# Kernel optimization log

Measured on AMD Instinct MI355X. Metric: run time of the kernel, lower is better.

The kernel has to match this reference:

```python
import jax, jax.numpy as jnp
import numpy as np

B = 8192      # batch (nodes)
HOPS = 15
SEQ = HOPS + 1
IN = 512      # input_dim
H = 256       # hidden_dim
DS = 64       # d_state
L = 6         # n_layers
NC = 40       # n_class
EPS = 1e-5


def _ln(x, g, b):
    m = x.mean(-1, keepdims=True)
    v = x.var(-1, keepdims=True)  # population var, matches torch LayerNorm
    return (x - m) / jnp.sqrt(v + EPS) * g + b


def setup_inputs() -> dict:
    key = jax.random.key(0)
    ks = jax.random.split(key, 16)
    n = lambda k, shp: jax.random.normal(k, shp, dtype=jnp.float32) * 0.02
    inp = {}
    inp["batched_data"] = jax.random.normal(ks[0], (B, SEQ, IN), dtype=jnp.float32)
    inp["in_w"] = n(ks[1], (H, IN)); inp["in_b"] = jnp.zeros((H,), jnp.float32)
    # per-layer stacked params (leading dim L); note: each MambaBlock shares ONE
    # LayerNorm instance for both pre-ssm and pre-ffn norm.
    inp["norm_g"] = jnp.ones((L, H), jnp.float32); inp["norm_b"] = jnp.zeros((L, H), jnp.float32)
    inp["A_w"] = n(ks[2], (L, DS, H))
    inp["B_w"] = n(ks[3], (L, DS, H))
    inp["C_w"] = n(ks[4], (L, H, DS))
    inp["D_w"] = n(ks[5], (L, H, H)); inp["D_b"] = jnp.zeros((L, H), jnp.float32)
    inp["gate_w"] = n(ks[6], (L, H, H)); inp["gate_b"] = jnp.zeros((L, H), jnp.float32)
    inp["ffn_w1"] = n(ks[7], (L, 2 * H, H)); inp["ffn_b1"] = jnp.zeros((L, 2 * H), jnp.float32)
    inp["ffn_w2"] = n(ks[8], (L, H, 2 * H)); inp["ffn_b2"] = jnp.zeros((L, H), jnp.float32)
    inp["fln_g"] = jnp.ones((H,), jnp.float32); inp["fln_b"] = jnp.zeros((H,), jnp.float32)
    inp["out_w"] = n(ks[9], (H // 2, H)); inp["out_b"] = jnp.zeros((H // 2,), jnp.float32)
    inp["cls_w"] = n(ks[10], (NC, H // 2)); inp["cls_b"] = jnp.zeros((NC,), jnp.float32)
    inp["attn_w"] = n(ks[11], (1, 2 * H)); inp["attn_b"] = jnp.zeros((1,), jnp.float32)
    return inp


def reference(batched_data, in_w, in_b, norm_g, norm_b, A_w, B_w, C_w, D_w, D_b,
              gate_w, gate_b, ffn_w1, ffn_b1, ffn_w2, ffn_b2, fln_g, fln_b,
              out_w, out_b, cls_w, cls_b, attn_w, attn_b):
    x = batched_data @ in_w.T + in_b  # [B,S,H]

    def layer(x, p):
        ng, nb, Aw, Bw, Cw, Dw, Db, gw, gb, w1, b1, w2, b2 = p
        y = _ln(x, ng, nb)
        # precompute all per-step projections in batched GEMMs
        a = jnp.tanh(jnp.einsum('bsh,dh->bsd', y, Aw))   # [B,S,DS]
        bt = jnp.einsum('bsh,dh->bsd', y, Bw)            # [B,S,DS]
        g = jax.nn.sigmoid(y @ gw.T + gb)                # [B,S,H]
        dt = y @ Dw.T + Db                               # [B,S,H]

        def step(h, ab):
            at, bbt = ab
            h = at * h + bbt
            return h, h

        h0 = jnp.zeros((x.shape[0], Aw.shape[0]), x.dtype)
        _, hs = jax.lax.scan(step, h0, (a.transpose(1, 0, 2), bt.transpose(1, 0, 2)))  # [S,B,DS]
        ys = jnp.einsum('sbd,hd->bsh', hs, Cw)           # [B,S,H]
        x = x + ys * g + dt * (1.0 - g)
        y = _ln(x, ng, nb)  # same norm params (shared LayerNorm in block)
        y = jax.nn.gelu(y @ w1.T + b1, approximate=False) @ w2.T + b2
        return x + y, None

    x, _ = jax.lax.scan(layer, x, (norm_g, norm_b, A_w, B_w, C_w, D_w, D_b,
                                   gate_w, gate_b, ffn_w1, ffn_b1, ffn_w2, ffn_b2))
    x = _ln(x, fln_g, fln_b)
    node = x[:, :1, :]           # [B,1,H]
    nbr = x[:, 1:, :]            # [B,S-1,H]
    ai = jnp.concatenate([jnp.broadcast_to(node, nbr.shape), nbr], axis=2)  # [B,S-1,2H]
    aw = jax.nn.softmax(ai @ attn_w.T + attn_b, axis=1)  # [B,S-1,1]
    agg = jnp.sum(nbr * aw, axis=1, keepdims=True)
    out = (node + agg)[:, 0, :]
    out = jax.nn.relu(out @ out_w.T + out_b) @ cls_w.T + cls_b
    return jax.nn.log_softmax(out, axis=1)
```

## Files before the change

### kernel.cpp

```cpp
#include <hip/hip_runtime.h>

typedef __attribute__((ext_vector_type(8))) short bf16x8_t;
typedef __attribute__((ext_vector_type(4))) float f32x4_t;

__device__ __forceinline__ ushort f2bf(float x) {
  union { float f; unsigned u; } a; a.f = x;
  unsigned r = a.u + 0x7fffu + ((a.u >> 16) & 1u);
  return (ushort)(r >> 16);
}
__device__ __forceinline__ float bf2f(ushort s) {
  union { unsigned u; float f; } a; a.u = ((unsigned)s) << 16;
  return a.f;
}
__device__ __forceinline__ void gload_lds16(const void* g, void* l) {
  __builtin_amdgcn_global_load_lds(
      (const __attribute__((address_space(1))) unsigned int*)g,
      (__attribute__((address_space(3))) unsigned int*)l, 16, 0, 0);
}
__device__ __forceinline__ int swzkey(int r) { return ((r >> 2) ^ r) & 3; }

__global__ void cvt_kernel(const float* __restrict__ s, ushort* __restrict__ d, int n) {
  int i = blockIdx.x * 256 + threadIdx.x;
  if (i < n) d[i] = f2bf(s[i]);
}

__global__ void build_wcat(const float* __restrict__ Aw, const float* __restrict__ Bw,
                           const float* __restrict__ gw, const float* __restrict__ Dw,
                           ushort* __restrict__ out) {
  int i = blockIdx.x * 256 + threadIdx.x;
  if (i >= 6 * 640 * 256) return;
  int l = i / (640 * 256), r = (i / 256) % 640, c = i % 256;
  float v;
  if (r < 64)        v = Aw[((l * 64 + r) * 256) + c];
  else if (r < 128)  v = Bw[((l * 64 + (r - 64)) * 256) + c];
  else if (r < 384)  v = gw[((l * 256 + (r - 128)) * 256) + c];
  else               v = Dw[((l * 256 + (r - 384)) * 256) + c];
  out[i] = f2bf(v);
}

__global__ void repack_gen(const ushort* __restrict__ src, ushort* __restrict__ dst,
                           int K, int perMat, int dstPerMat, int dstOff, long total) {
  const long i = (long)blockIdx.x * 256 + threadIdx.x;
  if (i >= total) return;
  const int m = (int)(i / perMat);
  const int idx = (int)(i % perMat);
  const int slice = idx >> 12;
  const int ksn = K >> 5;
  const int p = slice / ksn, ks = slice - p * ksn;
  const int r = (idx >> 5) & 127;
  const int s = (idx >> 3) & 3;
  const int e = idx & 7;
  const int k = ks * 32 + ((s ^ ((r >> 1) & 3)) << 3) + e;
  dst[(long)m * dstPerMat + dstOff + idx] = src[(long)m * perMat + (p * 128 + r) * K + k];
}

__global__ __launch_bounds__(256, 3)
void mamba_fused(ushort* __restrict__ y, ushort* __restrict__ xP,
                 const ushort* __restrict__ Wk,
                 const float* __restrict__ gb, const float* __restrict__ db,
                 const float* __restrict__ lng, const float* __restrict__ lnb) {
  __shared__ __align__(16) char WsB[2 * 16384];
  __shared__ __align__(16) ushort ab[32 * 136];
  __shared__ __align__(16) char HsB[4096];
  __shared__ float lsum[32][2], lsq[32][2];

  const int t = threadIdx.x, lane = t & 63, wid = t >> 6;
  const long m0 = (long)blockIdx.x * 32;
  const int wr = (wid >> 1) * 16, wc = (wid & 1) * 64;
  const int co4 = wid * 4;
  const char* Wb = (const char*)Wk;

  const int krow = lane & 15, kslot = lane >> 4;
  const int ar = wr + krow;

  bf16x8_t afr[8];
  {
    const char* yrow = (const char*)y + (m0 + ar) * 512 + kslot * 16;
#pragma unroll
    for (int ks = 0; ks < 8; ++ks) afr[ks] = *(const bf16x8_t*)(yrow + ks * 64);
  }
#pragma unroll
  for (int c = 0; c < 4; ++c)
    gload_lds16(Wb + (co4 + c) * 1024 + lane * 16, WsB + (co4 + c) * 1024);

  int boff[4];
#pragma unroll
  for (int i = 0; i < 4; ++i) {
    const int br = wc + i * 16 + krow;
    boff[i] = br * 64 + ((kslot ^ ((br >> 1) & 3)) << 4);
  }
  const int rbase = (lane >> 4) * 4, cbase = lane & 15;

  const f32x4_t zero = {0.f, 0.f, 0.f, 0.f};
  f32x4_t acc[4];
#pragma unroll
  for (int i = 0; i < 4; ++i) acc[i] = zero;

  int pair = 0;
  auto kstep2 = [&](bf16x8_t afa, bf16x8_t afb) {
    __syncthreads();
    if (pair + 1 < 22) {
      const char* src = Wb + (long)(pair + 1) * 16384;
      char* dst = WsB + ((pair + 1) & 1) * 16384;
#pragma unroll
      for (int c = 0; c < 4; ++c)
        gload_lds16(src + (co4 + c) * 1024 + lane * 16, dst + (co4 + c) * 1024);
    }
    const char* Wc = WsB + (pair & 1) * 16384;
    bf16x8_t bva[4], bvb[4];
#pragma unroll
    for (int i = 0; i < 4; ++i) bva[i] = *(const bf16x8_t*)(Wc + boff[i]);
#pragma unroll
    for (int i = 0; i < 4; ++i) bvb[i] = *(const bf16x8_t*)(Wc + 8192 + boff[i]);
    __builtin_amdgcn_s_setprio(1);
#pragma unroll
    for (int ni = 0; ni < 4; ++ni)
      acc[ni] = __builtin_amdgcn_mfma_f32_16x16x32_bf16(afa, bva[ni], acc[ni], 0, 0, 0);
#pragma unroll
    for (int ni = 0; ni < 4; ++ni)
      acc[ni] = __builtin_amdgcn_mfma_f32_16x16x32_bf16(afb, bvb[ni], acc[ni], 0, 0, 0);
    __builtin_amdgcn_s_setprio(0);
    ++pair;
  };

#pragma unroll
  for (int p = 0; p < 4; ++p) kstep2(afr[2 * p], afr[2 * p + 1]);
#pragma unroll
  for (int ni = 0; ni < 4; ++ni) {
    const int col = wc + ni * 16 + cbase;
#pragma unroll
    for (int j = 0; j < 4; ++j) {
      const int row = wr + rbase + j;
      const float v = acc[ni][j];
      ab[row * 136 + col] = f2bf(col < 64 ? tanhf(v) : v);
    }
    acc[ni] = zero;
  }
  __syncthreads();
  if (t < 128) {
    const int b = t >> 6, d = t & 63;
    float av[16], btv[16];
#pragma unroll
    for (int s = 0; s < 16; ++s) {
      const int row = b * 16 + s;
      av[s]  = bf2f(ab[row * 136 + d]);
      btv[s] = bf2f(ab[row * 136 + 64 + d]);
    }
    float h = 0.f;
#pragma unroll
    for (int s = 0; s < 16; ++s) {
      h = fmaf(av[s], h, btv[s]);
      const int row = b * 16 + s;
      *(ushort*)(HsB + row * 128 + (((d >> 3) ^ (row & 7)) << 4) + (d & 7) * 2) = f2bf(h);
    }
  }

  f32x4_t gsv[2][4], dsv[2][4], xnv[2][4];
#pragma unroll
  for (int pp = 0; pp < 2; ++pp) {
#pragma unroll
    for (int p = 0; p < 4; ++p) kstep2(afr[2 * p], afr[2 * p + 1]);
#pragma unroll
    for (int ni = 0; ni < 4; ++ni) {
      const int col = pp * 128 + wc + ni * 16 + cbase;
#pragma unroll
      for (int j = 0; j < 4; ++j) {
        const float s = acc[ni][j] + gb[col];
        gsv[pp][ni][j] = 1.f / (1.f + expf(-s));
      }
      acc[ni] = zero;
    }
  }
#pragma unroll
  for (int pp = 0; pp < 2; ++pp) {
#pragma unroll
    for (int p = 0; p < 4; ++p) kstep2(afr[2 * p], afr[2 * p + 1]);
#pragma unroll
    for (int ni = 0; ni < 4; ++ni) {
      const int col = pp * 128 + wc + ni * 16 + cbase;
#pragma unroll
      for (int j = 0; j < 4; ++j) dsv[pp][ni][j] = acc[ni][j] + db[col];
      acc[ni] = zero;
    }
  }
  const long rq16 = (m0 >> 4) + (wr >> 4);
#pragma unroll
  for (int pp = 0; pp < 2; ++pp) {
    const bf16x8_t afh0 = *(const bf16x8_t*)(
        HsB + (ar << 7) + ((kslot ^ (ar & 7)) << 4));
    const bf16x8_t afh1 = *(const bf16x8_t*)(
        HsB + (ar << 7) + (((4 | kslot) ^ (ar & 7)) << 4));
    kstep2(afh0, afh1);
#pragma unroll
    for (int ni = 0; ni < 4; ++ni) {
      const int colq = pp * 8 + (wid & 1) * 4 + ni;
      const ushort4 x4 = *(const ushort4*)(xP + (rq16 * 16 + colq) * 256 + lane * 4);
#pragma unroll
      for (int j = 0; j < 4; ++j) {
        const float g = gsv[pp][ni][j], dv = dsv[pp][ni][j];
        const float xo = bf2f(j == 0 ? x4.x : (j == 1 ? x4.y : (j == 2 ? x4.z : x4.w)));
        xnv[pp][ni][j] = xo + acc[ni][j] * g + dv * (1.f - g);
      }
      acc[ni] = zero;
    }
  }
#pragma unroll
  for (int j = 0; j < 4; ++j) {
    float ps = 0.f, pq = 0.f;
#pragma unroll
    for (int pp = 0; pp < 2; ++pp)
#pragma unroll
      for (int ni = 0; ni < 4; ++ni) { const float v = xnv[pp][ni][j]; ps += v; pq += v * v; }
#pragma unroll
    for (int off = 1; off < 16; off <<= 1) {
      ps += __shfl_xor(ps, off, 64);
      pq += __shfl_xor(pq, off, 64);
    }
    if ((lane & 15) == 0) {
      const int row = wr + rbase + j;
      lsum[row][wid & 1] = ps;
      lsq[row][wid & 1] = pq;
    }
  }
  __syncthreads();
#pragma unroll
  for (int pp = 0; pp < 2; ++pp) {
#pragma unroll
    for (int ni = 0; ni < 4; ++ni) {
      const int colq = pp * 8 + (wid & 1) * 4 + ni;
      ushort4 o4;
      o4.x = f2bf(xnv[pp][ni][0]);
      o4.y = f2bf(xnv[pp][ni][1]);
      o4.z = f2bf(xnv[pp][ni][2]);
      o4.w = f2bf(xnv[pp][ni][3]);
      *(ushort4*)(xP + (rq16 * 16 + colq) * 256 + lane * 4) = o4;
    }
  }
#pragma unroll
  for (int j = 0; j < 4; ++j) {
    const int row = wr + rbase + j;
    const float sm = lsum[row][0] + lsum[row][1];
    const float q = lsq[row][0] + lsq[row][1];
    const float mean = sm * (1.f / 256.f);
    const float rstd = rsqrtf(q * (1.f / 256.f) - mean * mean + 1e-5f);
#pragma unroll
    for (int pp = 0; pp < 2; ++pp)
#pragma unroll
      for (int ni = 0; ni < 4; ++ni) {
        const int col = pp * 128 + wc + ni * 16 + cbase;
        *(ushort*)(WsB + row * 512 + col * 2) =
            f2bf((xnv[pp][ni][j] - mean) * rstd * lng[col] + lnb[col]);
      }
  }
  __syncthreads();
#pragma unroll
  for (int rr = 0; rr < 4; ++rr) {
    const int byte = rr * 4096 + t * 16;
    const int row = byte >> 9, off = byte & 511;
    const bf16x8_t v = *(const bf16x8_t*)(WsB + byte);
    *(bf16x8_t*)((char*)y + (m0 + row) * 512 + off) = v;
  }
}

template <int NP, int MODE>
__global__ __launch_bounds__(256)
void gemm_ws(const ushort* __restrict__ A, const ushort* __restrict__ Wks,
             const float* __restrict__ b1, ushort* __restrict__ outp) {
  constexpr int KS = 8;
  constexpr int N = NP * 128;
  constexpr int T = NP * KS;
  __shared__ __align__(16) char AsB[128 * 512];

  const int t = threadIdx.x, lane = t & 63, wid = t >> 6;
  const long m0 = (long)blockIdx.x * 128;
  const int wr = (wid >> 1) * 64, wc = (wid & 1) * 64;
  const char* Ab = (const char*)A;
  const char* Wb = (const char*)Wks;

  {
    const int arow = lane >> 5;
    const int aps  = lane & 31;
#pragma unroll
    for (int j = 0; j < 16; ++j) {
      const int r = j * 8 + wid * 2 + arow;
      gload_lds16(Ab + (m0 + r) * 512 + (long)((aps ^ (r & 7)) << 4),
                  AsB + (j * 8 + wid * 2) * 512);
    }
  }

  const int krow = lane & 15, kslot = lane >> 4;
  int abase[4], akey[4], boff[4];
#pragma unroll
  for (int i = 0; i < 4; ++i) {
    const int ar = wr + i * 16 + krow;
    abase[i] = ar * 512;
    akey[i] = ar & 7;
    const int br = wc + i * 16 + krow;
    boff[i] = br * 64 + ((kslot ^ ((br >> 1) & 3)) << 4);
  }

  const f32x4_t zero = {0.f, 0.f, 0.f, 0.f};
  f32x4_t acc[4][4];
#pragma unroll
  for (int i = 0; i < 4; ++i)
#pragma unroll
    for (int j = 0; j < 4; ++j) acc[i][j] = zero;

  const int rbase = (lane >> 4) * 4, cbase = lane & 15;

  __syncthreads();

  bf16x8_t bv[4];
#pragma unroll
  for (int i = 0; i < 4; ++i) bv[i] = *(const bf16x8_t*)(Wb + boff[i]);

  for (int tau = 0; tau < T; ++tau) {
    bf16x8_t bw[4];
    if (tau + 1 < T) {
      const char* src = Wb + (long)(tau + 1) * 8192;
#pragma unroll
      for (int i = 0; i < 4; ++i) bw[i] = *(const bf16x8_t*)(src + boff[i]);
    } else {
#pragma unroll
      for (int i = 0; i < 4; ++i) bw[i] = bv[i];
    }
    const int ks = tau & 7;
    bf16x8_t af[4];
#pragma unroll
    for (int i = 0; i < 4; ++i)
      af[i] = *(const bf16x8_t*)(AsB + abase[i] + ((((ks << 2) | kslot) ^ akey[i]) << 4));
    __builtin_amdgcn_s_setprio(1);
#pragma unroll
    for (int mi = 0; mi < 4; ++mi)
#pragma unroll
      for (int ni = 0; ni < 4; ++ni)
        acc[mi][ni] = __builtin_amdgcn_mfma_f32_16x16x32_bf16(af[mi], bv[ni], acc[mi][ni], 0, 0, 0);
    __builtin_amdgcn_s_setprio(0);
#pragma unroll
    for (int i = 0; i < 4; ++i) bv[i] = bw[i];

    if (ks == KS - 1) {
      const int np = tau >> 3;
#pragma unroll
      for (int mi = 0; mi < 4; ++mi) {
#pragma unroll
        for (int ni = 0; ni < 4; ++ni) {
          const int col = np * 128 + wc + ni * 16 + cbase;
#pragma unroll
          for (int j = 0; j < 4; ++j) {
            const long row = m0 + wr + mi * 16 + rbase + j;
            float s = acc[mi][ni][j] + b1[col];
            float o;
            if constexpr (MODE == 2) o = 0.5f * s * (1.f + erff(s * 0.70710678118654752f));
            else                     o = fmaxf(s, 0.f);
            outp[row * N + col] = f2bf(o);
          }
          acc[mi][ni] = zero;
        }
      }
    }
  }
}

template <int K, int MODE, bool AFP32>
__global__ __launch_bounds__(512)
void gemm_ln(const void* __restrict__ Ap, const ushort* __restrict__ W,
             const float* __restrict__ b1, ushort* __restrict__ xP,
             const float* __restrict__ lng, const float* __restrict__ lnb,
             ushort* __restrict__ y, int writex) {
  constexpr int KS = K / 32;
  __shared__ __align__(16) char WsB[2 * 16384];
  __shared__ __align__(16) char AsB[2 * 8192];
  __shared__ float lsum4[128][4], lsq4[128][4];

  const int t = threadIdx.x, lane = t & 63, wid = t >> 6;
  const int wr = (wid >> 2) * 64, wc = (wid & 3) * 64;
  const int lr = lane >> 2, lc = lane & 3;
  const int ra = wid * 16 + lr;
  const int slog = lc ^ swzkey(ra);
  const int saA = slog << 4;
  const int rw0 = wid * 32 + lr, rw1 = rw0 + 16;
  const int sw0 = (lc ^ swzkey(rw0)) << 4;
  const int sw1 = (lc ^ swzkey(rw1)) << 4;
  const char* Ab = (const char*)Ap;
  const char* Wb = (const char*)W;
  constexpr long K2 = (long)K * 2;
  const long m0 = (long)blockIdx.x * 128;

  auto stageA = [&](int tau2) {
    char* dst = AsB + (tau2 & 1) * 8192 + wid * 1024 + lane * 16;
    if constexpr (AFP32) {
      const float* src = (const float*)Ap + (m0 + ra) * K + tau2 * 32 + slog * 8;
      const float4 q0 = ((const float4*)src)[0];
      const float4 q1 = ((const float4*)src)[1];
      bf16x8_t v;
      v[0] = (short)f2bf(q0.x); v[1] = (short)f2bf(q0.y);
      v[2] = (short)f2bf(q0.z); v[3] = (short)f2bf(q0.w);
      v[4] = (short)f2bf(q1.x); v[5] = (short)f2bf(q1.y);
      v[6] = (short)f2bf(q1.z); v[7] = (short)f2bf(q1.w);
      *(bf16x8_t*)dst = v;
    } else {
      gload_lds16(Ab + (m0 + ra) * K2 + (long)tau2 * 64 + saA,
                  AsB + (tau2 & 1) * 8192 + wid * 1024);
    }
  };

  gload_lds16(Wb + (long)rw0 * K2 + sw0, WsB + wid * 2048);
  gload_lds16(Wb + (long)rw1 * K2 + sw1, WsB + wid * 2048 + 1024);
  stageA(0);

  const int krow = lane & 15, kslot = lane >> 4;
  int aoff[4], boff[4];
#pragma unroll
  for (int i = 0; i < 4; ++i) {
    int ar = wr + i * 16 + krow;
    aoff[i] = ar * 64 + ((kslot ^ swzkey(ar)) << 4);
    int br = wc + i * 16 + krow;
    boff[i] = br * 64 + ((kslot ^ swzkey(br)) << 4);
  }

  const f32x4_t zero = {0.f, 0.f, 0.f, 0.f};
  f32x4_t acc[4][4];
#pragma unroll
  for (int i = 0; i < 4; ++i)
#pragma unroll
    for (int j = 0; j < 4; ++j) acc[i][j] = zero;

  for (int tau = 0; tau < KS; ++tau) {
    __syncthreads();
    if (tau + 1 < KS) {
      stageA(tau + 1);
      const long kb = (long)(tau + 1) * 64;
      char* wd = WsB + ((tau + 1) & 1) * 16384 + wid * 2048;
      gload_lds16(Wb + (long)rw0 * K2 + kb + sw0, wd);
      gload_lds16(Wb + (long)rw1 * K2 + kb + sw1, wd + 1024);
    }
    const char* Ac = AsB + (tau & 1) * 8192;
    const char* Wc = WsB + (tau & 1) * 16384;
    bf16x8_t af[4], bv[4];
#pragma unroll
    for (int i = 0; i < 4; ++i) af[i] = *(const bf16x8_t*)(Ac + aoff[i]);
#pragma unroll
    for (int i = 0; i < 4; ++i) bv[i] = *(const bf16x8_t*)(Wc + boff[i]);
#pragma unroll
    for (int mi = 0; mi < 4; ++mi)
#pragma unroll
      for (int ni = 0; ni < 4; ++ni)
        acc[mi][ni] = __builtin_amdgcn_mfma_f32_16x16x32_bf16(af[mi], bv[ni], acc[mi][ni], 0, 0, 0);
  }

  const int rbase = (lane >> 4) * 4;
  const int cbase = lane & 15;
  const long xbB = (long)blockIdx.x * 32768;
#pragma unroll
  for (int mi = 0; mi < 4; ++mi) {
    const int rq = (wid >> 2) * 4 + mi;
#pragma unroll
    for (int ni = 0; ni < 4; ++ni) {
      const int col = wc + ni * 16 + cbase;
      const int cq = (wid & 3) * 4 + ni;
      ushort4 x4;
      if constexpr (MODE == 3) x4 = *(const ushort4*)(xP + xbB + ((rq * 16 + cq) * 64 + lane) * 4);
#pragma unroll
      for (int j = 0; j < 4; ++j) {
        float v = acc[mi][ni][j] + b1[col];
        if constexpr (MODE == 3)
          v += bf2f(j == 0 ? x4.x : (j == 1 ? x4.y : (j == 2 ? x4.z : x4.w)));
        acc[mi][ni][j] = v;
      }
    }
  }
#pragma unroll
  for (int mi = 0; mi < 4; ++mi) {
#pragma unroll
    for (int j = 0; j < 4; ++j) {
      float ps = 0.f, pq = 0.f;
#pragma unroll
      for (int ni = 0; ni < 4; ++ni) { float v = acc[mi][ni][j]; ps += v; pq += v * v; }
#pragma unroll
      for (int off = 1; off < 16; off <<= 1) {
        ps += __shfl_xor(ps, off, 64);
        pq += __shfl_xor(pq, off, 64);
      }
      if ((lane & 15) == 0) {
        int r = wr + mi * 16 + (lane >> 4) * 4 + j;
        lsum4[r][wid & 3] = ps;
        lsq4[r][wid & 3] = pq;
      }
    }
  }
  __syncthreads();
#pragma unroll
  for (int mi = 0; mi < 4; ++mi) {
    const int rq = (wid >> 2) * 4 + mi;
#pragma unroll
    for (int ni = 0; ni < 4; ++ni) {
      const int cq = (wid & 3) * 4 + ni;
      if (writex) {
        ushort4 o4;
        o4.x = f2bf(acc[mi][ni][0]);
        o4.y = f2bf(acc[mi][ni][1]);
        o4.z = f2bf(acc[mi][ni][2]);
        o4.w = f2bf(acc[mi][ni][3]);
        *(ushort4*)(xP + xbB + ((rq * 16 + cq) * 64 + lane) * 4) = o4;
      }
    }
  }
#pragma unroll
  for (int mi = 0; mi < 4; ++mi) {
#pragma unroll
    for (int j = 0; j < 4; ++j) {
      const int r = wr + mi * 16 + rbase + j;
      const float s = lsum4[r][0] + lsum4[r][1] + lsum4[r][2] + lsum4[r][3];
      const float q = lsq4[r][0] + lsq4[r][1] + lsq4[r][2] + lsq4[r][3];
      const float mean = s * (1.f / 256.f);
      const float rstd = rsqrtf(q * (1.f / 256.f) - mean * mean + 1e-5f);
      const long row = m0 + r;
#pragma unroll
      for (int ni = 0; ni < 4; ++ni) {
        const int col = wc + ni * 16 + cbase;
        y[row * 256 + col] = f2bf((acc[mi][ni][j] - mean) * rstd * lng[col] + lnb[col]);
      }
    }
  }
}

__global__ __launch_bounds__(256)
void head_agg(const ushort* __restrict__ y, const float* __restrict__ attw,
              ushort* __restrict__ vb) {
  const int t = threadIdx.x, lane = t & 63, w = t >> 6;
  const long b = (long)blockIdx.x * 4 + w;
  const ushort* yb = y + b * 16 * 256;
  const float4 w2 = *(const float4*)(attw + 256 + lane * 4);

  float4 rows[16];
  float lg[16];
#pragma unroll
  for (int r = 0; r < 16; ++r) {
    const ushort4 u = *(const ushort4*)(yb + r * 256 + lane * 4);
    float4 v4;
    v4.x = bf2f(u.x); v4.y = bf2f(u.y); v4.z = bf2f(u.z); v4.w = bf2f(u.w);
    rows[r] = v4;
    if (r >= 1) {
      float s = v4.x * w2.x + v4.y * w2.y + v4.z * w2.z + v4.w * w2.w;
#pragma unroll
      for (int off = 32; off > 0; off >>= 1) s += __shfl_xor(s, off, 64);
      lg[r] = s;
    }
  }
  float mx = -1e30f;
#pragma unroll
  for (int r = 1; r < 16; ++r) mx = fmaxf(mx, lg[r]);
  float den = 0.f;
#pragma unroll
  for (int r = 1; r < 16; ++r) { lg[r] = expf(lg[r] - mx); den += lg[r]; }
  const float inv = 1.f / den;
  float4 v = rows[0];
#pragma unroll
  for (int r = 1; r < 16; ++r) {
    const float a = lg[r] * inv;
    v.x += a * rows[r].x; v.y += a * rows[r].y;
    v.z += a * rows[r].z; v.w += a * rows[r].w;
  }
  ushort4 o;
  o.x = f2bf(v.x); o.y = f2bf(v.y); o.z = f2bf(v.z); o.w = f2bf(v.w);
  *(ushort4*)(vb + b * 256 + lane * 4) = o;
}

__global__ __launch_bounds__(256)
void head_cls(const ushort* __restrict__ o1b, const float* __restrict__ cw,
              const float* __restrict__ cb, float* __restrict__ out) {
  __shared__ float lw[4][40];
  const int t = threadIdx.x, lane = t & 63, w = t >> 6;
  const long b = (long)blockIdx.x * 4 + w;
  const ushort2 u = *(const ushort2*)(o1b + b * 128 + lane * 2);
  const float o1x = bf2f(u.x), o1y = bf2f(u.y);

#pragma unroll
  for (int o = 0; o < 40; ++o) {
    const float2 c = *(const float2*)(cw + o * 128 + lane * 2);
    float p = o1x * c.x + o1y * c.y;
#pragma unroll
    for (int off = 32; off > 0; off >>= 1) p += __shfl_xor(p, off, 64);
    if (lane == 0) lw[w][o] = p + cb[o];
  }
  const float v = (lane < 40) ? lw[w][lane] : -1e30f;
  float mx = v;
#pragma unroll
  for (int off = 32; off > 0; off >>= 1) mx = fmaxf(mx, __shfl_xor(mx, off, 64));
  float e = (lane < 40) ? expf(v - mx) : 0.f;
  float den = e;
#pragma unroll
  for (int off = 32; off > 0; off >>= 1) den += __shfl_xor(den, off, 64);
  if (lane < 40) out[b * 40 + lane] = v - mx - logf(den);
}

extern "C" void kernel_launch(void* const* d_in, const int* in_sizes, int n_in,
                              void* d_out, int out_size, void* d_ws, size_t ws_size,
                              hipStream_t stream) {
  const float* data   = (const float*)d_in[0];
  const float* in_w   = (const float*)d_in[1];
  const float* in_b   = (const float*)d_in[2];
  const float* norm_g = (const float*)d_in[3];
  const float* norm_b = (const float*)d_in[4];
  const float* A_w    = (const float*)d_in[5];
  const float* B_w    = (const float*)d_in[6];
  const float* C_w    = (const float*)d_in[7];
  const float* D_w    = (const float*)d_in[8];
  const float* D_b    = (const float*)d_in[9];
  const float* gate_w = (const float*)d_in[10];
  const float* gate_b = (const float*)d_in[11];
  const float* ffn_w1 = (const float*)d_in[12];
  const float* ffn_b1 = (const float*)d_in[13];
  const float* ffn_w2 = (const float*)d_in[14];
  const float* ffn_b2 = (const float*)d_in[15];
  const float* fln_g  = (const float*)d_in[16];
  const float* fln_b  = (const float*)d_in[17];
  const float* out_w  = (const float*)d_in[18];
  const float* out_b  = (const float*)d_in[19];
  const float* cls_w  = (const float*)d_in[20];
  const float* cls_b  = (const float*)d_in[21];
  const float* attn_w = (const float*)d_in[22];
  const float* attn_b = (const float*)d_in[23];
  (void)in_sizes; (void)n_in; (void)out_size; (void)ws_size; (void)attn_b;

  char* ws = (char*)d_ws;
  ushort* xP     = (ushort*)(ws + 0);
  ushort* y      = (ushort*)(ws + 67108864);
  ushort* tzp    = (ushort*)(ws + 134217728);
  ushort* wcat   = (ushort*)(ws + 318767104);
  ushort* inwb   = (ushort*)(ws + 320733184);
  ushort* w1b    = (ushort*)(ws + 320995328);
  ushort* w2b    = (ushort*)(ws + 322568192);
  ushort* cwb    = (ushort*)(ws + 324141056);
  ushort* mslice = (ushort*)(ws + 324337664);
  ushort* w1k    = (ushort*)(ws + 326500352);
  ushort* owb    = (ushort*)(ws + 328073216);
  ushort* owk    = (ushort*)(ws + 328138752);
  ushort* vb     = tzp;
  ushort* o1b    = tzp + 2097152;

  cvt_kernel<<<512, 256, 0, stream>>>(in_w, inwb, 131072);
  cvt_kernel<<<3072, 256, 0, stream>>>(ffn_w1, w1b, 786432);
  cvt_kernel<<<3072, 256, 0, stream>>>(ffn_w2, w2b, 786432);
  cvt_kernel<<<384, 256, 0, stream>>>(C_w, cwb, 98304);
  cvt_kernel<<<128, 256, 0, stream>>>(out_w, owb, 32768);
  build_wcat<<<3840, 256, 0, stream>>>(A_w, B_w, gate_w, D_w, wcat);
  repack_gen<<<3840, 256, 0, stream>>>(wcat, mslice, 256, 163840, 180224, 0, 6L * 163840);
  repack_gen<<<384, 256, 0, stream>>>(cwb, mslice, 64, 16384, 180224, 163840, 6L * 16384);
  repack_gen<<<3072, 256, 0, stream>>>(w1b, w1k, 256, 131072, 131072, 0, 6L * 131072);
  repack_gen<<<128, 256, 0, stream>>>(owb, owk, 256, 32768, 32768, 0, 32768);

  gemm_ln<512, 0, true><<<dim3(1024), 512, 0, stream>>>(
      data, inwb, in_b, xP, norm_g, norm_b, y, 1);

  for (int l = 0; l < 6; ++l) {
    mamba_fused<<<4096, 256, 0, stream>>>(
        y, xP, mslice + (size_t)l * 180224,
        gate_b + l * 256, D_b + l * 256, norm_g + l * 256, norm_b + l * 256);
    gemm_ws<4, 2><<<1024, 256, 0, stream>>>(
        y, w1k + (size_t)l * 131072, ffn_b1 + l * 512, tzp);
    const float* lg2 = (l < 5) ? (norm_g + (l + 1) * 256) : fln_g;
    const float* lb2 = (l < 5) ? (norm_b + (l + 1) * 256) : fln_b;
    gemm_ln<512, 3, false><<<dim3(1024), 512, 0, stream>>>(
        tzp, w2b + (size_t)l * 256 * 512, ffn_b2 + l * 256, xP, lg2, lb2, y, (l < 5) ? 1 : 0);
  }

  head_agg<<<2048, 256, 0, stream>>>(y, attn_w, vb);
  gemm_ws<1, 3><<<64, 256, 0, stream>>>(vb, owk, out_b, o1b);
  head_cls<<<2048, 256, 0, stream>>>(o1b, cls_w, cls_b, (float*)d_out);
}
```

Baseline: 2.110 ms.

## Fuse FFN up-projection, GELU and down-projection with residual LayerNorm in one kernel

Replaces the two FFN launches per layer (up GEMM writing a bf16 intermediate to global memory, then a down GEMM with residual and LayerNorm) with one kernel. Each block handles 32 rows and keeps the GELU intermediate in LDS, so the 2H-wide activation never goes to HBM. Weights are read straight from global memory in a pre-swizzled layout, which needs an extra repack pass for W2. The costs are small row tiles, so each block re-reads all the weights from L2, and no LDS staging of B, which may lower MFMA efficiency.

```diff
diff --git a/kernel.cpp b/kernel.cpp
--- a/kernel.cpp
+++ b/kernel.cpp
@@ -258,6 +258,184 @@
     const int byte = rr * 4096 + t * 16;
     const int row = byte >> 9, off = byte & 511;
     const bf16x8_t v = *(const bf16x8_t*)(WsB + byte);
+    *(bf16x8_t*)((char*)y + (m0 + row) * 512 + off) = v;
+  }
+}
+
+__global__ __launch_bounds__(256, 3)
+void ffn_fused2(ushort* __restrict__ y, ushort* __restrict__ xP,
+                const ushort* __restrict__ W1k, const ushort* __restrict__ W2k,
+                const float* __restrict__ b1, const float* __restrict__ b2,
+                const float* __restrict__ lng, const float* __restrict__ lnb,
+                int writex) {
+  __shared__ __align__(16) char Ts[32768];
+  __shared__ float lsum[32][2], lsq[32][2];
+
+  const int t = threadIdx.x, lane = t & 63, wid = t >> 6;
+  const long m0 = (long)blockIdx.x * 32;
+  const int wr = (wid >> 1) * 16, wc = (wid & 1) * 64;
+  const int krow = lane & 15, kslot = lane >> 4;
+  const int ar = wr + krow;
+  const int rbase = (lane >> 4) * 4, cbase = lane & 15;
+
+  bf16x8_t afr[8];
+  {
+    const char* yrow = (const char*)y + (m0 + ar) * 512 + kslot * 16;
+#pragma unroll
+    for (int ks = 0; ks < 8; ++ks) afr[ks] = *(const bf16x8_t*)(yrow + ks * 64);
+  }
+
+  int boff[4];
+#pragma unroll
+  for (int i = 0; i < 4; ++i) {
+    const int br = wc + i * 16 + krow;
+    boff[i] = br * 64 + ((kslot ^ ((br >> 1) & 3)) << 4);
+  }
+
+  const f32x4_t zero = {0.f, 0.f, 0.f, 0.f};
+  f32x4_t acc[4];
+#pragma unroll
+  for (int i = 0; i < 4; ++i) acc[i] = zero;
+
+  const char* W1 = (const char*)W1k;
+  bf16x8_t bv[4];
+#pragma unroll
+  for (int i = 0; i < 4; ++i) bv[i] = *(const bf16x8_t*)(W1 + boff[i]);
+  for (int np = 0; np < 4; ++np) {
+#pragma unroll
+    for (int ks = 0; ks < 8; ++ks) {
+      const int sl = np * 8 + ks;
+      bf16x8_t bw[4];
+      if (sl + 1 < 32) {
+        const char* src = W1 + (long)(sl + 1) * 8192;
+#pragma unroll
+        for (int i = 0; i < 4; ++i) bw[i] = *(const bf16x8_t*)(src + boff[i]);
+      } else {
+#pragma unroll
+        for (int i = 0; i < 4; ++i) bw[i] = bv[i];
+      }
+      __builtin_amdgcn_s_setprio(1);
+#pragma unroll
+      for (int ni = 0; ni < 4; ++ni)
+        acc[ni] = __builtin_amdgcn_mfma_f32_16x16x32_bf16(afr[ks], bv[ni], acc[ni], 0, 0, 0);
+      __builtin_amdgcn_s_setprio(0);
+#pragma unroll
+      for (int i = 0; i < 4; ++i) bv[i] = bw[i];
+    }
+#pragma unroll
+    for (int ni = 0; ni < 4; ++ni) {
+      const int col = np * 128 + wc + ni * 16 + cbase;
+      const int slog = col >> 3;
+#pragma unroll
+      for (int j = 0; j < 4; ++j) {
+        const int row = wr + rbase + j;
+        const float s = acc[ni][j] + b1[col];
+        const float o = 0.5f * s * (1.f + erff(s * 0.70710678118654752f));
+        *(ushort*)(Ts + row * 1024 + ((slog ^ (row & 7)) << 4) + (col & 7) * 2) = f2bf(o);
+      }
+      acc[ni] = zero;
+    }
+  }
+  __syncthreads();
+
+  const char* W2 = (const char*)W2k;
+  f32x4_t xnv[2][4];
+  const long rq16 = (m0 >> 4) + (wr >> 4);
+  bf16x8_t bv2[4];
+#pragma unroll
+  for (int i = 0; i < 4; ++i) bv2[i] = *(const bf16x8_t*)(W2 + boff[i]);
+  for (int pp = 0; pp < 2; ++pp) {
+#pragma unroll
+    for (int ks = 0; ks < 16; ++ks) {
+      const int sl = pp * 16 + ks;
+      bf16x8_t bw[4];
+      if (sl + 1 < 32) {
+        const char* src = W2 + (long)(sl + 1) * 8192;
+#pragma unroll
+        for (int i = 0; i < 4; ++i) bw[i] = *(const bf16x8_t*)(src + boff[i]);
+      } else {
+#pragma unroll
+        for (int i = 0; i < 4; ++i) bw[i] = bv2[i];
+      }
+      const bf16x8_t af = *(const bf16x8_t*)(
+          Ts + ar * 1024 + (((ks * 4 + kslot) ^ (ar & 7)) << 4));
+      __builtin_amdgcn_s_setprio(1);
+#pragma unroll
+      for (int ni = 0; ni < 4; ++ni)
+        acc[ni] = __builtin_amdgcn_mfma_f32_16x16x32_bf16(af, bv2[ni], acc[ni], 0, 0, 0);
+      __builtin_amdgcn_s_setprio(0);
+#pragma unroll
+      for (int i = 0; i < 4; ++i) bv2[i] = bw[i];
+    }
+#pragma unroll
+    for (int ni = 0; ni < 4; ++ni) {
+      const int colq = pp * 8 + (wid & 1) * 4 + ni;
+      const int col = pp * 128 + wc + ni * 16 + cbase;
+      const ushort4 x4 = *(const ushort4*)(xP + (rq16 * 16 + colq) * 256 + lane * 4);
+#pragma unroll
+      for (int j = 0; j < 4; ++j) {
+        const float xo = bf2f(j == 0 ? x4.x : (j == 1 ? x4.y : (j == 2 ? x4.z : x4.w)));
+        xnv[pp][ni][j] = xo + acc[ni][j] + b2[col];
+      }
+      acc[ni] = zero;
+    }
+  }
+#pragma unroll
+  for (int j = 0; j < 4; ++j) {
+    float ps = 0.f, pq = 0.f;
+#pragma unroll
+    for (int pp = 0; pp < 2; ++pp)
+#pragma unroll
+      for (int ni = 0; ni < 4; ++ni) { const float v = xnv[pp][ni][j]; ps += v; pq += v * v; }
+#pragma unroll
+    for (int off = 1; off < 16; off <<= 1) {
+      ps += __shfl_xor(ps, off, 64);
+      pq += __shfl_xor(pq, off, 64);
+    }
+    if ((lane & 15) == 0) {
+      const int row = wr + rbase + j;
+      lsum[row][wid & 1] = ps;
+      lsq[row][wid & 1] = pq;
+    }
+  }
+  __syncthreads();
+  if (writex) {
+#pragma unroll
+    for (int pp = 0; pp < 2; ++pp) {
+#pragma unroll
+      for (int ni = 0; ni < 4; ++ni) {
+        const int colq = pp * 8 + (wid & 1) * 4 + ni;
+        ushort4 o4;
+        o4.x = f2bf(xnv[pp][ni][0]);
+        o4.y = f2bf(xnv[pp][ni][1]);
+        o4.z = f2bf(xnv[pp][ni][2]);
+        o4.w = f2bf(xnv[pp][ni][3]);
+        *(ushort4*)(xP + (rq16 * 16 + colq) * 256 + lane * 4) = o4;
+      }
+    }
+  }
+#pragma unroll
+  for (int j = 0; j < 4; ++j) {
+    const int row = wr + rbase + j;
+    const float sm = lsum[row][0] + lsum[row][1];
+    const float q = lsq[row][0] + lsq[row][1];
+    const float mean = sm * (1.f / 256.f);
+    const float rstd = rsqrtf(q * (1.f / 256.f) - mean * mean + 1e-5f);
+#pragma unroll
+    for (int pp = 0; pp < 2; ++pp)
+#pragma unroll
+      for (int ni = 0; ni < 4; ++ni) {
+        const int col = pp * 128 + wc + ni * 16 + cbase;
+        *(ushort*)(Ts + row * 512 + col * 2) =
+            f2bf((xnv[pp][ni][j] - mean) * rstd * lng[col] + lnb[col]);
+      }
+  }
+  __syncthreads();
+#pragma unroll
+  for (int rr = 0; rr < 4; ++rr) {
+    const int byte = rr * 4096 + t * 16;
+    const int row = byte >> 9, off = byte & 511;
+    const bf16x8_t v = *(const bf16x8_t*)(Ts + byte);
     *(bf16x8_t*)((char*)y + (m0 + row) * 512 + off) = v;
   }
 }
@@ -637,6 +815,7 @@
   ushort* w1k    = (ushort*)(ws + 326500352);
   ushort* owb    = (ushort*)(ws + 328073216);
   ushort* owk    = (ushort*)(ws + 328138752);
+  ushort* w2k    = (ushort*)(ws + 328204288);
   ushort* vb     = tzp;
   ushort* o1b    = tzp + 2097152;
 
@@ -649,6 +828,7 @@
   repack_gen<<<3840, 256, 0, stream>>>(wcat, mslice, 256, 163840, 180224, 0, 6L * 163840);
   repack_gen<<<384, 256, 0, stream>>>(cwb, mslice, 64, 16384, 180224, 163840, 6L * 16384);
   repack_gen<<<3072, 256, 0, stream>>>(w1b, w1k, 256, 131072, 131072, 0, 6L * 131072);
+  repack_gen<<<3072, 256, 0, stream>>>(w2b, w2k, 512, 131072, 131072, 0, 6L * 131072);
   repack_gen<<<128, 256, 0, stream>>>(owb, owk, 256, 32768, 32768, 0, 32768);
 
   gemm_ln<512, 0, true><<<dim3(1024), 512, 0, stream>>>(
@@ -658,12 +838,11 @@
     mamba_fused<<<4096, 256, 0, stream>>>(
         y, xP, mslice + (size_t)l * 180224,
         gate_b + l * 256, D_b + l * 256, norm_g + l * 256, norm_b + l * 256);
-    gemm_ws<4, 2><<<1024, 256, 0, stream>>>(
-        y, w1k + (size_t)l * 131072, ffn_b1 + l * 512, tzp);
     const float* lg2 = (l < 5) ? (norm_g + (l + 1) * 256) : fln_g;
     const float* lb2 = (l < 5) ? (norm_b + (l + 1) * 256) : fln_b;
-    gemm_ln<512, 3, false><<<dim3(1024), 512, 0, stream>>>(
-        tzp, w2b + (size_t)l * 256 * 512, ffn_b2 + l * 256, xP, lg2, lb2, y, (l < 5) ? 1 : 0);
+    ffn_fused2<<<4096, 256, 0, stream>>>(
+        y, xP, w1k + (size_t)l * 131072, w2k + (size_t)l * 131072,
+        ffn_b1 + l * 512, ffn_b2 + l * 256, lg2, lb2, (l < 5) ? 1 : 0);
   }
 
   head_agg<<<2048, 256, 0, stream>>>(y, attn_w, vb);
```

After: 1.983 ms, median of 2. -6.0%, faster.
